# Optimization experiments

Hardware: AMD Instinct MI355X
Metric: run time of the kernel (lower is better)

Reference implementation:

```python
import jax, jax.numpy as jnp
import numpy as np

EPS = 1e-6


def setup_inputs() -> dict:
    key = jax.random.key(0)
    k1, k2, k3, k4, k5 = jax.random.split(key, 5)
    B, L, K, NFG, NH, NFO = 4, 1024, 32, 4, 16, 32
    return {
        "beta": jax.random.normal(k1, (B, L, NFG * NH), dtype=jnp.float32),
        "self_attention": jax.random.normal(k2, (B, L, NFG * NH), dtype=jnp.float32),
        "attn_coef": jax.random.normal(k3, (B, L, K, NFG * NH), dtype=jnp.float32),
        "node_out": jax.random.normal(k4, (B, L, K, NFO * NH), dtype=jnp.float32),
        "graph_weights": jax.random.uniform(k5, (B, L, K, NFG), dtype=jnp.float32),
    }


def reference(beta, self_attention, attn_coef, node_out, graph_weights):
    B, L, K, nfg = graph_weights.shape
    nh = attn_coef.shape[-1] // nfg
    nfo = node_out.shape[-1] // nh

    beta = beta.reshape(B, L, nfg, nh)
    sa = self_attention.reshape(B, L, nfg, nh)
    ac = attn_coef.reshape(B, L, K, nfg, nh)
    no = node_out.reshape(B, L, K, nfo, nh)

    # add self-attention term to the first (self) neighbor slot
    ac = ac.at[:, :, 0].add(sa)
    # beta gating, broadcast over neighbors
    ac = ac * (beta[:, :, None] + EPS)
    # stabilized exp over (K, nfg) jointly
    ac = ac - jnp.max(ac, axis=(-3, -2), keepdims=True)
    weighted = jnp.exp(ac) * graph_weights[..., None]          # [B,L,K,nfg,nh]
    attn_final = jnp.sum(weighted, axis=-2)                    # [B,L,K,nh]
    attn_final = attn_final / (jnp.sum(jnp.abs(attn_final), axis=-2, keepdims=True) + EPS)
    # weighted aggregation over neighbors
    output = jnp.einsum("blkfh,blkh->blfh", no, attn_final).reshape(B, L, nfo * nh)
    return output, attn_final
```

## Files before the change

### kernel.cpp

```cpp
#include <hip/hip_runtime.h>

#define EPS 1e-6f

constexpr int KNB = 32;
constexpr int NFG = 4;
constexpr int NH  = 16;
constexpr int NFO = 32;
constexpr int FH  = NFG * NH;
constexpr int ACN = KNB * FH;
constexpr int ON  = NFO * NH;
constexpr int KN  = KNB * NH;

__global__ __launch_bounds__(256, 4)
void attn_fused(const float* __restrict__ beta,
                const float* __restrict__ sa,
                const float* __restrict__ ac,
                const float* __restrict__ no,
                const float* __restrict__ gw,
                float* __restrict__ out,
                float* __restrict__ attn_out)
{
    const int bl   = blockIdx.x;
    const int tid  = threadIdx.x;
    const int lane = tid & 63;
    const int wv   = tid >> 6;

    __shared__ float s_ac[ACN];
    __shared__ float s_attn[KN];
    __shared__ float s_gw[KNB * NFG];
    __shared__ float s_bg[FH];
    __shared__ float s_wm[4 * NH];
    __shared__ float s_wd[4 * NH];
    __shared__ float s_part[ON];

    const size_t blz = (size_t)bl;
    const float* acp = ac + blz * ACN;
    const float* nop = no + blz * (size_t)(KNB * ON);

    if (tid < FH)        s_bg[tid] = beta[blz * FH + tid] + EPS;
    if (tid < KNB * NFG) s_gw[tid] = gw[blz * (KNB * NFG) + tid];
    __syncthreads();

    const int h = tid & 15;

    float lmax = -INFINITY;
    #pragma unroll
    for (int j = 0; j < 8; ++j) {
        const int idx = tid + j * 256;
        float v = acp[idx];
        if (j == 0 && tid < FH) v += sa[blz * FH + tid];
        v *= s_bg[idx & 63];
        s_ac[idx] = v;
        lmax = fmaxf(lmax, v);
    }

    lmax = fmaxf(lmax, __shfl_xor(lmax, 16, 64));
    lmax = fmaxf(lmax, __shfl_xor(lmax, 32, 64));
    if (lane < 16) s_wm[wv * 16 + lane] = lmax;
    __syncthreads();
    const float m = fmaxf(fmaxf(s_wm[h], s_wm[16 + h]),
                          fmaxf(s_wm[32 + h], s_wm[48 + h]));

    const int k0 = tid >> 4;
    float a0 = 0.f, a1 = 0.f;
    #pragma unroll
    for (int f = 0; f < NFG; ++f) {
        a0 += __expf(s_ac[k0 * 64 + f * 16 + h] - m)        * s_gw[k0 * 4 + f];
        a1 += __expf(s_ac[(k0 + 16) * 64 + f * 16 + h] - m) * s_gw[(k0 + 16) * 4 + f];
    }

    float ls = fabsf(a0) + fabsf(a1);
    ls += __shfl_xor(ls, 16, 64);
    ls += __shfl_xor(ls, 32, 64);
    if (lane < 16) s_wd[wv * 16 + lane] = ls;
    __syncthreads();
    const float den = s_wd[h] + s_wd[16 + h] + s_wd[32 + h] + s_wd[48 + h] + EPS;

    const float n0 = a0 / den;
    const float n1 = a1 / den;
    s_attn[tid]       = n0;
    s_attn[tid + 256] = n1;
    attn_out[blz * KN + tid]       = n0;
    attn_out[blz * KN + tid + 256] = n1;
    __syncthreads();

    const int half = tid >> 7;
    const int u    = tid & 127;
    const int p    = u * 4;
    const float* basep = nop + half * ON + p;
    float4 acc = make_float4(0.f, 0.f, 0.f, 0.f);
    #pragma unroll 8
    for (int j = 0; j < 16; ++j) {
        const float4 v = *reinterpret_cast<const float4*>(basep + j * 1024);
        const float4 w = *reinterpret_cast<const float4*>(
            &s_attn[(2 * j + half) * 16 + (p & 15)]);
        acc.x += v.x * w.x;
        acc.y += v.y * w.y;
        acc.z += v.z * w.z;
        acc.w += v.w * w.w;
    }
    if (half) {
        *reinterpret_cast<float4*>(&s_part[p]) = acc;
    }
    __syncthreads();
    if (!half) {
        const float4 q = *reinterpret_cast<const float4*>(&s_part[p]);
        acc.x += q.x; acc.y += q.y; acc.z += q.z; acc.w += q.w;
        *reinterpret_cast<float4*>(out + blz * ON + p) = acc;
    }
}

extern "C" void kernel_launch(void* const* d_in, const int* in_sizes, int n_in,
                              void* d_out, int out_size, void* d_ws, size_t ws_size,
                              hipStream_t stream) {
    const float* beta = (const float*)d_in[0];
    const float* sa   = (const float*)d_in[1];
    const float* ac   = (const float*)d_in[2];
    const float* no   = (const float*)d_in[3];
    const float* gw   = (const float*)d_in[4];

    const int BL = in_sizes[0] / FH;
    float* out      = (float*)d_out;
    float* attn_out = out + (size_t)BL * ON;

    attn_fused<<<BL, 256, 0, stream>>>(beta, sa, ac, no, gw, out, attn_out);
}
```

Measured before the change: 388.3 us.

## Prefetch node_out before softmax and stream it through a register ring

The first eight neighbor rows of node_out are loaded into registers before the softmax reduction, so that memory traffic overlaps the exp and normalization work. The aggregation is restructured so each thread owns two output columns across all 32 neighbors, with an 8-deep register ring buffer, which removes the split-half partial sum and its extra barrier. The beta and graph_weights shared-memory staging and its barrier are also replaced by direct per-thread register loads. The cost is higher register pressure, plus 8-byte loads in place of 16-byte ones.

```diff
diff --git a/kernel.cpp b/kernel.cpp
--- a/kernel.cpp
+++ b/kernel.cpp
@@ -27,21 +27,19 @@
 
     __shared__ float s_ac[ACN];
     __shared__ float s_attn[KN];
-    __shared__ float s_gw[KNB * NFG];
-    __shared__ float s_bg[FH];
     __shared__ float s_wm[4 * NH];
     __shared__ float s_wd[4 * NH];
-    __shared__ float s_part[ON];
 
     const size_t blz = (size_t)bl;
     const float* acp = ac + blz * ACN;
     const float* nop = no + blz * (size_t)(KNB * ON);
 
-    if (tid < FH)        s_bg[tid] = beta[blz * FH + tid] + EPS;
-    if (tid < KNB * NFG) s_gw[tid] = gw[blz * (KNB * NFG) + tid];
-    __syncthreads();
+    const int h  = tid & 15;
+    const int k0 = tid >> 4;
 
-    const int h = tid & 15;
+    const float4 gw0 = *reinterpret_cast<const float4*>(gw + blz * (KNB * NFG) + k0 * 4);
+    const float4 gw1 = *reinterpret_cast<const float4*>(gw + blz * (KNB * NFG) + (k0 + 16) * 4);
+    const float bg = beta[blz * FH + (tid & 63)] + EPS;
 
     float lmax = -INFINITY;
     #pragma unroll
@@ -49,10 +47,18 @@
         const int idx = tid + j * 256;
         float v = acp[idx];
         if (j == 0 && tid < FH) v += sa[blz * FH + tid];
-        v *= s_bg[idx & 63];
+        v *= bg;
         s_ac[idx] = v;
         lmax = fmaxf(lmax, v);
     }
+
+    const int p2 = tid * 2;
+    const int hp = p2 & 15;
+    const float* npp = nop + p2;
+    float2 v[8];
+    #pragma unroll
+    for (int k = 0; k < 8; ++k)
+        v[k] = *reinterpret_cast<const float2*>(npp + k * ON);
 
     lmax = fmaxf(lmax, __shfl_xor(lmax, 16, 64));
     lmax = fmaxf(lmax, __shfl_xor(lmax, 32, 64));
@@ -61,13 +67,16 @@
     const float m = fmaxf(fmaxf(s_wm[h], s_wm[16 + h]),
                           fmaxf(s_wm[32 + h], s_wm[48 + h]));
 
-    const int k0 = tid >> 4;
-    float a0 = 0.f, a1 = 0.f;
-    #pragma unroll
-    for (int f = 0; f < NFG; ++f) {
-        a0 += __expf(s_ac[k0 * 64 + f * 16 + h] - m)        * s_gw[k0 * 4 + f];
-        a1 += __expf(s_ac[(k0 + 16) * 64 + f * 16 + h] - m) * s_gw[(k0 + 16) * 4 + f];
-    }
+    const float* r0 = s_ac + k0 * 64 + h;
+    float a0 = __expf(r0[ 0] - m) * gw0.x
+             + __expf(r0[16] - m) * gw0.y
+             + __expf(r0[32] - m) * gw0.z
+             + __expf(r0[48] - m) * gw0.w;
+    const float* r1 = s_ac + (k0 + 16) * 64 + h;
+    float a1 = __expf(r1[ 0] - m) * gw1.x
+             + __expf(r1[16] - m) * gw1.y
+             + __expf(r1[32] - m) * gw1.z
+             + __expf(r1[48] - m) * gw1.w;
 
     float ls = fabsf(a0) + fabsf(a1);
     ls += __shfl_xor(ls, 16, 64);
@@ -84,30 +93,17 @@
     attn_out[blz * KN + tid + 256] = n1;
     __syncthreads();
 
-    const int half = tid >> 7;
-    const int u    = tid & 127;
-    const int p    = u * 4;
-    const float* basep = nop + half * ON + p;
-    float4 acc = make_float4(0.f, 0.f, 0.f, 0.f);
-    #pragma unroll 8
-    for (int j = 0; j < 16; ++j) {
-        const float4 v = *reinterpret_cast<const float4*>(basep + j * 1024);
-        const float4 w = *reinterpret_cast<const float4*>(
-            &s_attn[(2 * j + half) * 16 + (p & 15)]);
-        acc.x += v.x * w.x;
-        acc.y += v.y * w.y;
-        acc.z += v.z * w.z;
-        acc.w += v.w * w.w;
+    float2 acc = make_float2(0.f, 0.f);
+    #pragma unroll
+    for (int k = 0; k < KNB; ++k) {
+        const float2 w = *reinterpret_cast<const float2*>(&s_attn[k * 16 + hp]);
+        const float2 x = v[k & 7];
+        if (k < KNB - 8)
+            v[k & 7] = *reinterpret_cast<const float2*>(npp + (k + 8) * ON);
+        acc.x += x.x * w.x;
+        acc.y += x.y * w.y;
     }
-    if (half) {
-        *reinterpret_cast<float4*>(&s_part[p]) = acc;
-    }
-    __syncthreads();
-    if (!half) {
-        const float4 q = *reinterpret_cast<const float4*>(&s_part[p]);
-        acc.x += q.x; acc.y += q.y; acc.z += q.z; acc.w += q.w;
-        *reinterpret_cast<float4*>(out + blz * ON + p) = acc;
-    }
+    *reinterpret_cast<float2*>(out + blz * ON + p2) = acc;
 }
 
 extern "C" void kernel_launch(void* const* d_in, const int* in_sizes, int n_in,
```

Result: no change. 388.4 us (+0.0%).
